# Optimization experiments

Measured on AMD Instinct MI355X. Metric: run time of the kernel, lower is better.

## Reference

```python
import jax, jax.numpy as jnp
import numpy as np

N_NODES = 50000
N_EDGES = 800000
DIM = 128
NEG_SLOPE = 0.2


def gat_conv(x, ei, W, a_src, a_dst, b):
    """PyG GATConv, heads=1, add_self_loops=True."""
    N = x.shape[0]
    h = x @ W  # [N, out]
    loop = jnp.arange(N, dtype=ei.dtype)
    src = jnp.concatenate([ei[0], loop])
    dst = jnp.concatenate([ei[1], loop])
    al = h @ a_src  # [N]
    ar = h @ a_dst  # [N]
    e = jax.nn.leaky_relu(al[src] + ar[dst], NEG_SLOPE)  # [E+N]
    m = jax.ops.segment_max(e, dst, num_segments=N)
    ex = jnp.exp(e - m[dst])
    s = jax.ops.segment_sum(ex, dst, num_segments=N)
    alpha = ex / s[dst]
    out = jax.ops.segment_sum(h[src] * alpha[:, None], dst, num_segments=N)
    return out + b


def setup_inputs() -> dict:
    key = jax.random.key(0)
    ks = jax.random.split(key, 32)
    sc = 1.0 / np.sqrt(DIM)
    inp = {"x": jax.random.normal(ks[0], (N_NODES, DIM), jnp.float32)}
    for i in range(5):
        inp[f"W{i+1}"] = jax.random.normal(ks[1 + 4 * i], (DIM, DIM), jnp.float32) * sc
        inp[f"as{i+1}"] = jax.random.normal(ks[2 + 4 * i], (DIM,), jnp.float32) * sc
        inp[f"ad{i+1}"] = jax.random.normal(ks[3 + 4 * i], (DIM,), jnp.float32) * sc
        inp[f"b{i+1}"] = jnp.zeros((DIM,), jnp.float32)
    inp["edge_index"] = jax.random.randint(ks[22], (2, N_EDGES), 0, N_NODES, jnp.int32)
    inp["edge_index_cross"] = jax.random.randint(ks[23], (2, N_EDGES), 0, N_NODES, jnp.int32)
    return inp


def reference(x, W1, as1, ad1, b1, W2, as2, ad2, b2, W3, as3, ad3, b3,
              W4, as4, ad4, b4, W5, as5, ad5, b5, edge_index, edge_index_cross):
    # dropout is identity in inference mode
    x = jax.nn.relu(gat_conv(x, edge_index, W1, as1, ad1, b1))
    x = jax.nn.relu(gat_conv(x, edge_index_cross, W2, as2, ad2, b2))
    x = jax.nn.relu(gat_conv(x, edge_index, W3, as3, ad3, b3))
    x = jax.nn.relu(gat_conv(x, edge_index_cross, W4, as4, ad4, b4))
    x = gat_conv(x, edge_index, W5, as5, ad5, b5)
    return jnp.squeeze(x)
```

## Files before the change

### kernel.cpp

```cpp
#include <hip/hip_runtime.h>

#define DIM 128
#define NEG 0.2f
#define CAP 128
#define BSZ 512
#define CB  256

typedef __attribute__((ext_vector_type(8))) short bf16x8;
typedef __attribute__((ext_vector_type(4))) float f32x4;
typedef __attribute__((ext_vector_type(8))) _Float16 h16x8;
typedef __attribute__((ext_vector_type(8))) unsigned short us8;

__device__ __forceinline__ float lrelu(float v) { return v > 0.f ? v : NEG * v; }

__device__ __forceinline__ unsigned short f2bf(float f) {
    unsigned u = __float_as_uint(f);
    unsigned r = (u + 0x7FFFu + ((u >> 16) & 1u)) >> 16;
    return (unsigned short)r;
}
__device__ __forceinline__ float bf2f(unsigned short h) {
    return __uint_as_float(((unsigned)h) << 16);
}


__global__ __launch_bounds__(256) void convert_x(const float* __restrict__ x,
                                                 unsigned short* __restrict__ hi,
                                                 unsigned short* __restrict__ lo, int n4) {
    int i = blockIdx.x * 256 + threadIdx.x;
    if (i >= n4) return;
    const int p = i * 4;
    const int tile = p >> 11, kc = (p >> 9) & 3, q = (p >> 7) & 3;
    const int rr = (p >> 3) & 15, j0 = p & 7;
    const int row = tile * 16 + rr;
    const int k = kc * 32 + q * 8 + j0;
    float4 v = *(const float4*)(x + (size_t)row * DIM + k);
    ushort4 h, l;
    h.x = f2bf(v.x); l.x = f2bf(v.x - bf2f(h.x));
    h.y = f2bf(v.y); l.y = f2bf(v.y - bf2f(h.y));
    h.z = f2bf(v.z); l.z = f2bf(v.z - bf2f(h.z));
    h.w = f2bf(v.w); l.w = f2bf(v.w - bf2f(h.w));
    *(ushort4*)(hi + p) = h;
    *(ushort4*)(lo + p) = l;
}

__global__ __launch_bounds__(256) void convert_w(const float* __restrict__ W,
                                                 unsigned short* __restrict__ Bhi,
                                                 unsigned short* __restrict__ Blo) {
    int i = blockIdx.x * 256 + threadIdx.x;
    if (i >= 16384) return;
    const int tt = i >> 11, kc = (i >> 9) & 3, q = (i >> 7) & 3;
    const int n = (i >> 3) & 15, j = i & 7;
    const int c = tt * 16 + n;
    const int k = kc * 32 + q * 8 + j;
    float v = W[k * 128 + c];
    unsigned short h = f2bf(v);
    Bhi[i] = h;
    Blo[i] = f2bf(v - bf2f(h));
}

__global__ __launch_bounds__(256) void gemm_mfma(const unsigned short* __restrict__ Ahi,
                                                 const unsigned short* __restrict__ Alo,
                                                 const unsigned short* __restrict__ Bhi,
                                                 const unsigned short* __restrict__ Blo,
                                                 const float* __restrict__ asrc,
                                                 const float* __restrict__ adst,
                                                 _Float16* __restrict__ Hh,
                                                 float* __restrict__ al,
                                                 float* __restrict__ ar, int N) {
    const int t = threadIdx.x;
    const int wv = t >> 6;
    const int l = t & 63;
    const int tile = blockIdx.x * 4 + wv;
    const int r0 = tile * 16;
    const int m = l & 15;
    const int q = l >> 4;

    f32x4 acc[8];
#pragma unroll
    for (int tt = 0; tt < 8; ++tt) acc[tt] = (f32x4){0.f, 0.f, 0.f, 0.f};

    const size_t abase = (size_t)tile * 2048 + (size_t)l * 8;
#pragma unroll
    for (int kc = 0; kc < 4; ++kc) {
        const bf16x8 ahi = *(const bf16x8*)(Ahi + abase + kc * 512);
        const bf16x8 alo = *(const bf16x8*)(Alo + abase + kc * 512);
#pragma unroll
        for (int tt = 0; tt < 8; ++tt) {
            const size_t boff = (size_t)tt * 2048 + kc * 512 + (size_t)l * 8;
            const bf16x8 bhi = *(const bf16x8*)(Bhi + boff);
            const bf16x8 blo = *(const bf16x8*)(Blo + boff);
            acc[tt] = __builtin_amdgcn_mfma_f32_16x16x32_bf16(ahi, bhi, acc[tt], 0, 0, 0);
            acc[tt] = __builtin_amdgcn_mfma_f32_16x16x32_bf16(ahi, blo, acc[tt], 0, 0, 0);
            acc[tt] = __builtin_amdgcn_mfma_f32_16x16x32_bf16(alo, bhi, acc[tt], 0, 0, 0);
        }
    }

#pragma unroll
    for (int j = 0; j < 4; ++j) {
        const int rr = r0 + q * 4 + j;
        if (rr < N) {
            _Float16* hp = Hh + (size_t)rr * DIM + m;
#pragma unroll
            for (int tt = 0; tt < 8; ++tt) hp[tt * 16] = (_Float16)acc[tt][j];
        }
    }

    float pa[4] = {0.f, 0.f, 0.f, 0.f};
    float pr[4] = {0.f, 0.f, 0.f, 0.f};
#pragma unroll
    for (int tt = 0; tt < 8; ++tt) {
        const float as = asrc[tt * 16 + m];
        const float ad = adst[tt * 16 + m];
#pragma unroll
        for (int j = 0; j < 4; ++j) {
            pa[j] += acc[tt][j] * as;
            pr[j] += acc[tt][j] * ad;
        }
    }
#pragma unroll
    for (int off = 8; off; off >>= 1) {
#pragma unroll
        for (int j = 0; j < 4; ++j) {
            pa[j] += __shfl_xor(pa[j], off);
            pr[j] += __shfl_xor(pr[j], off);
        }
    }
    if (m == 0) {
#pragma unroll
        for (int j = 0; j < 4; ++j) {
            const int rr = r0 + q * 4 + j;
            if (rr < N) { al[rr] = pa[j]; ar[rr] = pr[j]; }
        }
    }
}

__device__ __forceinline__ void edge_decode(int e, const int* ei, const int* eix,
                                            int E1, int N, int E2, int& src, int& d) {
    if (e < E1) {
        src = ei[e];
        d = ei[E1 + e];
    } else {
        int k = e - E1;
        src = eix[k];
        d = N + eix[E2 + k];
    }
}

__global__ __launch_bounds__(256) void csr_hist(const int* __restrict__ ei,
                                                const int* __restrict__ eix,
                                                int* __restrict__ g_hist,
                                                int E1, int E2, int N, int NB, int CE) {
    __shared__ int h[256];
    const int t = threadIdx.x;
    const int c = blockIdx.x;
    h[t] = 0;
    __syncthreads();
    const int Etot = E1 + E2;
    const int beg = c * CE;
    const int end = min(Etot, beg + CE);
    for (int e = beg + t; e < end; e += 256) {
        int src, d;
        edge_decode(e, ei, eix, E1, N, E2, src, d);
        atomicAdd(&h[d >> 9], 1);
    }
    __syncthreads();
    if (t < NB) g_hist[t * CB + c] = h[t];
}

__global__ __launch_bounds__(1024) void bsum_kernel(const int* __restrict__ in,
                                                    int* __restrict__ bsum, int L) {
    __shared__ int wsum[16];
    int t = threadIdx.x, wave = t >> 6, lane = t & 63;
    int i = blockIdx.x * 1024 + t;
    int v = (i < L) ? in[i] : 0;
#pragma unroll
    for (int off = 32; off; off >>= 1) v += __shfl_xor(v, off);
    if (lane == 0) wsum[wave] = v;
    __syncthreads();
    if (t == 0) {
        int s = 0;
#pragma unroll
        for (int j = 0; j < 16; ++j) s += wsum[j];
        bsum[blockIdx.x] = s;
    }
}

__global__ __launch_bounds__(128) void scan_small(int* __restrict__ bsum, int nb) {
    __shared__ int w0tot;
    int t = threadIdx.x;
    int v = (t < nb) ? bsum[t] : 0;
    int s = v;
#pragma unroll
    for (int off = 1; off < 64; off <<= 1) {
        int u = __shfl_up(s, off);
        if ((t & 63) >= off) s += u;
    }
    if (t == 63) w0tot = s;
    __syncthreads();
    if (t >= 64) s += w0tot;
    if (t < nb) bsum[t] = s - v;
}

__global__ __launch_bounds__(1024) void bscan_kernel(const int* __restrict__ in,
                                                     const int* __restrict__ bsum,
                                                     int* __restrict__ out, int L) {
    __shared__ int wsum[16];
    __shared__ int woff[16];
    int t = threadIdx.x, wave = t >> 6, lane = t & 63;
    int i = blockIdx.x * 1024 + t;
    int v = (i < L) ? in[i] : 0;
    int s = v;
#pragma unroll
    for (int off = 1; off < 64; off <<= 1) {
        int u = __shfl_up(s, off);
        if (lane >= off) s += u;
    }
    if (lane == 63) wsum[wave] = s;
    __syncthreads();
    if (t == 0) {
        int r = 0;
#pragma unroll
        for (int j = 0; j < 16; ++j) { woff[j] = r; r += wsum[j]; }
    }
    __syncthreads();
    if (i < L) out[i] = bsum[blockIdx.x] + woff[wave] + s - v;
}

__global__ __launch_bounds__(256) void csr_partition(const int* __restrict__ ei,
                                                     const int* __restrict__ eix,
                                                     const int* __restrict__ g_base,
                                                     unsigned* __restrict__ staging,
                                                     int E1, int E2, int N, int NB, int CE) {
    __shared__ int cur[256];
    const int t = threadIdx.x;
    const int c = blockIdx.x;
    if (t < NB) cur[t] = g_base[t * CB + c];
    __syncthreads();
    const int Etot = E1 + E2;
    const int beg = c * CE;
    const int end = min(Etot, beg + CE);
    for (int e = beg + t; e < end; e += 256) {
        int src, d;
        edge_decode(e, ei, eix, E1, N, E2, src, d);
        int p = atomicAdd(&cur[d >> 9], 1);
        staging[p] = ((unsigned)(d & (BSZ - 1)) << 22) | (unsigned)src;
    }
}

__global__ __launch_bounds__(256) void csr_finalize(const unsigned* __restrict__ staging,
                                                    const int* __restrict__ g_base,
                                                    int* __restrict__ row_off,
                                                    int* __restrict__ col,
                                                    int Ntot, int Etot, int NB) {
    __shared__ int cnt_s[BSZ];
    __shared__ int cur_s[BSZ];
    __shared__ int wsum[4], woff[4];
    const int t = threadIdx.x;
    const int k = blockIdx.x;
    cnt_s[t] = 0;
    cnt_s[t + 256] = 0;
    __syncthreads();
    const int seg_beg = g_base[k * CB];
    const int seg_end = (k == NB - 1) ? Etot : g_base[(k + 1) * CB];
    for (int i = seg_beg + t; i < seg_end; i += 256)
        atomicAdd(&cnt_s[staging[i] >> 22], 1);
    __syncthreads();

    const int a = cnt_s[2 * t], b = cnt_s[2 * t + 1];
    const int tsum = a + b;
    int s = tsum;
    const int lane = t & 63, wv = t >> 6;
#pragma unroll
    for (int off = 1; off < 64; off <<= 1) {
        int u = __shfl_up(s, off);
        if (lane >= off) s += u;
    }
    if (lane == 63) wsum[wv] = s;
    __syncthreads();
    if (t == 0) {
        int r = 0;
#pragma unroll
        for (int j = 0; j < 4; ++j) { woff[j] = r; r += wsum[j]; }
    }
    __syncthreads();
    const int excl = woff[wv] + s - tsum;
    cur_s[2 * t] = seg_beg + excl;
    cur_s[2 * t + 1] = seg_beg + excl + a;
    const int nbase = k * BSZ;
    if (nbase + 2 * t < Ntot)     row_off[nbase + 2 * t]     = seg_beg + excl;
    if (nbase + 2 * t + 1 < Ntot) row_off[nbase + 2 * t + 1] = seg_beg + excl + a;
    __syncthreads();
    for (int i = seg_beg + t; i < seg_end; i += 256) {
        unsigned v = staging[i];
        int p = atomicAdd(&cur_s[v >> 22], 1);
        col[p] = (int)(v & 0x3FFFFFu);
    }
    if (k == 0 && t == 0) row_off[Ntot] = Etot;
}

__global__ __launch_bounds__(256) void agg_kernel(const _Float16* __restrict__ Hh,
                                                  const float* __restrict__ al,
                                                  const float* __restrict__ ar,
                                                  const int* __restrict__ row_off,
                                                  const int* __restrict__ col,
                                                  const float* __restrict__ bias,
                                                  float* __restrict__ outF,
                                                  unsigned short* __restrict__ outHi,
                                                  unsigned short* __restrict__ outLo,
                                                  int N, int last) {
    __shared__ float salpha[16][CAP];
    __shared__ int   scol[16][CAP];
    const int t = threadIdx.x;
    const int wv = t >> 6;
    const int lane = t & 63;
    const int g = lane >> 4;
    const int j = lane & 15;
    const int slot = wv * 4 + g;
    const int w = blockIdx.x * 16 + slot;
    if (w >= N) return;

    const int beg = row_off[w];
    const int deg = row_off[w + 1] - beg;
    const float arn = ar[w];
    const float vself = lrelu(al[w] + arn);

    float mm = -1e30f, ss = 0.f;
    for (int i = j; i < deg; i += 16) {
        const int c = col[beg + i];
        float v = lrelu(al[c] + arn);
        if (i < CAP) { scol[slot][i] = c; salpha[slot][i] = v; }
        float nm = fmaxf(mm, v);
        ss = ss * __expf(mm - nm) + __expf(v - nm);
        mm = nm;
    }
#pragma unroll
    for (int off = 8; off; off >>= 1) {
        float mo = __shfl_xor(mm, off);
        float so = __shfl_xor(ss, off);
        float nm = fmaxf(mm, mo);
        ss = ss * __expf(mm - nm) + so * __expf(mo - nm);
        mm = nm;
    }
    {
        float nm = fmaxf(mm, vself);
        ss = ss * __expf(mm - nm) + __expf(vself - nm);
        mm = nm;
    }
    const float m = mm;
    const float invs = 1.f / ss;

    const int capdeg = deg < CAP ? deg : CAP;
    for (int i = j; i < capdeg; i += 16)
        salpha[slot][i] = __expf(salpha[slot][i] - m) * invs;

    const float aself = __expf(vself - m) * invs;
    const h16x8 hs = *(const h16x8*)(Hh + (size_t)w * DIM + 8 * j);
    float acc[8];
#pragma unroll
    for (int k = 0; k < 8; ++k) acc[k] = aself * (float)hs[k];

    int i = 0;
    for (; i + 3 < deg; i += 4) {
        int sn0, sn1, sn2, sn3;
        float a0, a1, a2, a3;
        if (i + 3 < CAP) {
            sn0 = scol[slot][i];     a0 = salpha[slot][i];
            sn1 = scol[slot][i + 1]; a1 = salpha[slot][i + 1];
            sn2 = scol[slot][i + 2]; a2 = salpha[slot][i + 2];
            sn3 = scol[slot][i + 3]; a3 = salpha[slot][i + 3];
        } else {
            const int e = beg + i;
            sn0 = col[e]; sn1 = col[e + 1]; sn2 = col[e + 2]; sn3 = col[e + 3];
            a0 = __expf(lrelu(al[sn0] + arn) - m) * invs;
            a1 = __expf(lrelu(al[sn1] + arn) - m) * invs;
            a2 = __expf(lrelu(al[sn2] + arn) - m) * invs;
            a3 = __expf(lrelu(al[sn3] + arn) - m) * invs;
        }
        const h16x8 h0 = *(const h16x8*)(Hh + (size_t)sn0 * DIM + 8 * j);
        const h16x8 h1 = *(const h16x8*)(Hh + (size_t)sn1 * DIM + 8 * j);
        const h16x8 h2 = *(const h16x8*)(Hh + (size_t)sn2 * DIM + 8 * j);
        const h16x8 h3 = *(const h16x8*)(Hh + (size_t)sn3 * DIM + 8 * j);
#pragma unroll
        for (int k = 0; k < 8; ++k)
            acc[k] += a0 * (float)h0[k] + a1 * (float)h1[k] +
                      a2 * (float)h2[k] + a3 * (float)h3[k];
    }
    for (; i < deg; ++i) {
        int sn;
        float a;
        if (i < CAP) {
            sn = scol[slot][i];
            a = salpha[slot][i];
        } else {
            sn = col[beg + i];
            a = __expf(lrelu(al[sn] + arn) - m) * invs;
        }
        const h16x8 hv = *(const h16x8*)(Hh + (size_t)sn * DIM + 8 * j);
#pragma unroll
        for (int k = 0; k < 8; ++k) acc[k] += a * (float)hv[k];
    }

    const float4 b0 = *(const float4*)(bias + 8 * j);
    const float4 b1 = *(const float4*)(bias + 8 * j + 4);
    float o[8];
    o[0] = acc[0] + b0.x; o[1] = acc[1] + b0.y;
    o[2] = acc[2] + b0.z; o[3] = acc[3] + b0.w;
    o[4] = acc[4] + b1.x; o[5] = acc[5] + b1.y;
    o[6] = acc[6] + b1.z; o[7] = acc[7] + b1.w;
    if (last) {
        float4 o0 = make_float4(o[0], o[1], o[2], o[3]);
        float4 o1 = make_float4(o[4], o[5], o[6], o[7]);
        *(float4*)(outF + (size_t)w * DIM + 8 * j) = o0;
        *(float4*)(outF + (size_t)w * DIM + 8 * j + 4) = o1;
    } else {
        us8 hv, lv;
#pragma unroll
        for (int k = 0; k < 8; ++k) {
            float v = fmaxf(o[k], 0.f);
            unsigned short hb = f2bf(v);
            hv[k] = hb;
            lv[k] = f2bf(v - bf2f(hb));
        }
        const size_t p = (size_t)(w >> 4) * 2048 +
                         (size_t)((j >> 2) * 512 + (j & 3) * 128 + (w & 15) * 8);
        *(us8*)(outHi + p) = hv;
        *(us8*)(outLo + p) = lv;
    }
}

extern "C" void kernel_launch(void* const* d_in, const int* in_sizes, int n_in,
                              void* d_out, int out_size, void* d_ws, size_t ws_size,
                              hipStream_t stream) {
    const float* x = (const float*)d_in[0];
    const float* W[5];
    const float* asv[5];
    const float* adv[5];
    const float* bv[5];
    for (int i = 0; i < 5; ++i) {
        W[i]   = (const float*)d_in[1 + 4 * i];
        asv[i] = (const float*)d_in[2 + 4 * i];
        adv[i] = (const float*)d_in[3 + 4 * i];
        bv[i]  = (const float*)d_in[4 + 4 * i];
    }
    const int* ei  = (const int*)d_in[21];
    const int* eix = (const int*)d_in[22];
    const int N  = in_sizes[0] / DIM;
    const int E1 = in_sizes[21] / 2;
    const int E2 = in_sizes[22] / 2;
    const int Ntot = 2 * N;
    const int Etot = E1 + E2;
    const int NB = (Ntot + BSZ - 1) / BSZ;
    const int CE = (Etot + CB - 1) / CB;
    const int gemm_blocks = (N + 63) / 64;
    const size_t tiles_alloc = (size_t)gemm_blocks * 4;

    size_t off = 0;
    auto alloc = [&](size_t bytes) {
        void* r = (char*)d_ws + off;
        off += (bytes + 255) & ~(size_t)255;
        return r;
    };
    float* Hbuf  = (float*)alloc((size_t)N * DIM * sizeof(float));
    unsigned short* Xhi = (unsigned short*)alloc(tiles_alloc * 2048 * 2);
    unsigned short* Xlo = (unsigned short*)alloc(tiles_alloc * 2048 * 2);
    float* al    = (float*)alloc((size_t)N * sizeof(float));
    float* ar    = (float*)alloc((size_t)N * sizeof(float));
    unsigned short* wthi = (unsigned short*)alloc(5 * 16384 * 2);
    unsigned short* wtlo = (unsigned short*)alloc(5 * 16384 * 2);
    int* g_hist  = (int*)alloc((size_t)NB * CB * sizeof(int));
    int* g_base  = (int*)alloc((size_t)NB * CB * sizeof(int));
    int* bsum    = (int*)alloc(128 * sizeof(int));
    int* row     = (int*)alloc((size_t)(Ntot + 1) * sizeof(int));
    int* col     = (int*)alloc((size_t)Etot * sizeof(int));
    (void)ws_size;
    unsigned* staging = (unsigned*)Hbuf;
    _Float16* Hh = (_Float16*)Hbuf;

    float* F = (float*)d_out;

    const int n4 = N * DIM / 4;
    convert_x<<<(n4 + 255) / 256, 256, 0, stream>>>(x, Xhi, Xlo, n4);
    for (int Lyr = 0; Lyr < 5; ++Lyr)
        convert_w<<<64, 256, 0, stream>>>(W[Lyr], wthi + Lyr * 16384, wtlo + Lyr * 16384);

    const int L = NB * CB;
    const int nbb = (L + 1023) / 1024;
    csr_hist<<<CB, 256, 0, stream>>>(ei, eix, g_hist, E1, E2, N, NB, CE);
    bsum_kernel<<<nbb, 1024, 0, stream>>>(g_hist, bsum, L);
    scan_small<<<1, 128, 0, stream>>>(bsum, nbb);
    bscan_kernel<<<nbb, 1024, 0, stream>>>(g_hist, bsum, g_base, L);
    csr_partition<<<CB, 256, 0, stream>>>(ei, eix, g_base, staging, E1, E2, N, NB, CE);
    csr_finalize<<<NB, 256, 0, stream>>>(staging, g_base, row, col, Ntot, Etot, NB);

    const int node_blocks = (N + 15) / 16;

    for (int Lyr = 0; Lyr < 5; ++Lyr) {
        gemm_mfma<<<gemm_blocks, 256, 0, stream>>>(Xhi, Xlo,
                                                   wthi + Lyr * 16384, wtlo + Lyr * 16384,
                                                   asv[Lyr], adv[Lyr], Hh, al, ar, N);
        const int* ro = row + ((Lyr % 2 == 0) ? 0 : N);
        agg_kernel<<<node_blocks, 256, 0, stream>>>(Hh, al, ar, ro, col, bv[Lyr],
                                                    F, Xhi, Xlo, N, (Lyr == 4) ? 1 : 0);
    }
}
```

Before: 444.6 us.

## Stage GEMM weights in LDS, degree-sort nodes for aggregation, batch weight conversion

The GEMM kernel now copies the split bf16 weight matrices into shared memory once per block and keeps the A fragments in registers, so B is no longer reread from global memory for every tile. A new bitonic sort reorders nodes by in-degree within each group of 256, and the aggregation kernel reads its node index through that permutation so the 16 nodes sharing a block have similar degrees and less divergence. The five weight-conversion launches are merged into one. The trade-offs are 64KB of LDS per GEMM block, which limits occupancy, two extra sort launches, and an indirection in the aggregation kernel that scatters its output writes.

```diff
diff --git a/kernel.cpp b/kernel.cpp
--- a/kernel.cpp
+++ b/kernel.cpp
@@ -43,19 +43,25 @@
     *(ushort4*)(lo + p) = l;
 }
 
-__global__ __launch_bounds__(256) void convert_w(const float* __restrict__ W,
+__global__ __launch_bounds__(256) void convert_w(const float* __restrict__ W0,
+                                                 const float* __restrict__ W1,
+                                                 const float* __restrict__ W2,
+                                                 const float* __restrict__ W3,
+                                                 const float* __restrict__ W4,
                                                  unsigned short* __restrict__ Bhi,
                                                  unsigned short* __restrict__ Blo) {
-    int i = blockIdx.x * 256 + threadIdx.x;
-    if (i >= 16384) return;
+    const int Lyr = blockIdx.x >> 6;
+    const float* W = (Lyr == 0) ? W0 : (Lyr == 1) ? W1 : (Lyr == 2) ? W2
+                    : (Lyr == 3) ? W3 : W4;
+    int i = (blockIdx.x & 63) * 256 + threadIdx.x;
     const int tt = i >> 11, kc = (i >> 9) & 3, q = (i >> 7) & 3;
     const int n = (i >> 3) & 15, j = i & 7;
     const int c = tt * 16 + n;
     const int k = kc * 32 + q * 8 + j;
     float v = W[k * 128 + c];
     unsigned short h = f2bf(v);
-    Bhi[i] = h;
-    Blo[i] = f2bf(v - bf2f(h));
+    Bhi[Lyr * 16384 + i] = h;
+    Blo[Lyr * 16384 + i] = f2bf(v - bf2f(h));
 }
 
 __global__ __launch_bounds__(256) void gemm_mfma(const unsigned short* __restrict__ Ahi,
@@ -67,6 +73,8 @@
                                                  _Float16* __restrict__ Hh,
                                                  float* __restrict__ al,
                                                  float* __restrict__ ar, int N) {
+    __shared__ unsigned short sBhi[16384];
+    __shared__ unsigned short sBlo[16384];
     const int t = threadIdx.x;
     const int wv = t >> 6;
     const int l = t & 63;
@@ -75,23 +83,40 @@
     const int m = l & 15;
     const int q = l >> 4;
 
+    bf16x8 ahi[4], alo[4];
+    const size_t abase = (size_t)tile * 2048 + (size_t)l * 8;
+#pragma unroll
+    for (int kc = 0; kc < 4; ++kc) {
+        ahi[kc] = *(const bf16x8*)(Ahi + abase + kc * 512);
+        alo[kc] = *(const bf16x8*)(Alo + abase + kc * 512);
+    }
+    {
+        const int4* gh = (const int4*)Bhi;
+        const int4* gl = (const int4*)Blo;
+        int4* sh = (int4*)sBhi;
+        int4* sl = (int4*)sBlo;
+#pragma unroll
+        for (int r = 0; r < 8; ++r) {
+            sh[t + 256 * r] = gh[t + 256 * r];
+            sl[t + 256 * r] = gl[t + 256 * r];
+        }
+    }
+    __syncthreads();
+
     f32x4 acc[8];
 #pragma unroll
     for (int tt = 0; tt < 8; ++tt) acc[tt] = (f32x4){0.f, 0.f, 0.f, 0.f};
 
-    const size_t abase = (size_t)tile * 2048 + (size_t)l * 8;
-#pragma unroll
-    for (int kc = 0; kc < 4; ++kc) {
-        const bf16x8 ahi = *(const bf16x8*)(Ahi + abase + kc * 512);
-        const bf16x8 alo = *(const bf16x8*)(Alo + abase + kc * 512);
-#pragma unroll
-        for (int tt = 0; tt < 8; ++tt) {
-            const size_t boff = (size_t)tt * 2048 + kc * 512 + (size_t)l * 8;
-            const bf16x8 bhi = *(const bf16x8*)(Bhi + boff);
-            const bf16x8 blo = *(const bf16x8*)(Blo + boff);
-            acc[tt] = __builtin_amdgcn_mfma_f32_16x16x32_bf16(ahi, bhi, acc[tt], 0, 0, 0);
-            acc[tt] = __builtin_amdgcn_mfma_f32_16x16x32_bf16(ahi, blo, acc[tt], 0, 0, 0);
-            acc[tt] = __builtin_amdgcn_mfma_f32_16x16x32_bf16(alo, bhi, acc[tt], 0, 0, 0);
+#pragma unroll
+    for (int tt = 0; tt < 8; ++tt) {
+#pragma unroll
+        for (int kc = 0; kc < 4; ++kc) {
+            const int boff = tt * 2048 + kc * 512 + l * 8;
+            const bf16x8 bhi = *(const bf16x8*)(sBhi + boff);
+            const bf16x8 blo = *(const bf16x8*)(sBlo + boff);
+            acc[tt] = __builtin_amdgcn_mfma_f32_16x16x32_bf16(ahi[kc], bhi, acc[tt], 0, 0, 0);
+            acc[tt] = __builtin_amdgcn_mfma_f32_16x16x32_bf16(ahi[kc], blo, acc[tt], 0, 0, 0);
+            acc[tt] = __builtin_amdgcn_mfma_f32_16x16x32_bf16(alo[kc], bhi, acc[tt], 0, 0, 0);
         }
     }
 
@@ -298,11 +323,39 @@
     if (k == 0 && t == 0) row_off[Ntot] = Etot;
 }
 
+__global__ __launch_bounds__(256) void sort_nodes(const int* __restrict__ row_off,
+                                                  int* __restrict__ perm, int N) {
+    __shared__ int kdeg[256];
+    __shared__ int kidx[256];
+    const int t = threadIdx.x;
+    const int w = blockIdx.x * 256 + t;
+    kdeg[t] = (w < N) ? (row_off[w + 1] - row_off[w]) : -1;
+    kidx[t] = w;
+    __syncthreads();
+#pragma unroll
+    for (int ksz = 2; ksz <= 256; ksz <<= 1) {
+        for (int jj = ksz >> 1; jj > 0; jj >>= 1) {
+            const int ixj = t ^ jj;
+            if (ixj > t) {
+                const int d0 = kdeg[t], d1 = kdeg[ixj];
+                const bool up = ((t & ksz) == 0);
+                if ((d0 > d1) == up) {
+                    kdeg[t] = d1; kdeg[ixj] = d0;
+                    const int i0 = kidx[t]; kidx[t] = kidx[ixj]; kidx[ixj] = i0;
+                }
+            }
+            __syncthreads();
+        }
+    }
+    perm[blockIdx.x * 256 + t] = kidx[t];
+}
+
 __global__ __launch_bounds__(256) void agg_kernel(const _Float16* __restrict__ Hh,
                                                   const float* __restrict__ al,
                                                   const float* __restrict__ ar,
                                                   const int* __restrict__ row_off,
                                                   const int* __restrict__ col,
+                                                  const int* __restrict__ perm,
                                                   const float* __restrict__ bias,
                                                   float* __restrict__ outF,
                                                   unsigned short* __restrict__ outHi,
@@ -316,7 +369,7 @@
     const int g = lane >> 4;
     const int j = lane & 15;
     const int slot = wv * 4 + g;
-    const int w = blockIdx.x * 16 + slot;
+    const int w = perm[blockIdx.x * 16 + slot];
     if (w >= N) return;
 
     const int beg = row_off[w];
@@ -453,6 +506,8 @@
     const int CE = (Etot + CB - 1) / CB;
     const int gemm_blocks = (N + 63) / 64;
     const size_t tiles_alloc = (size_t)gemm_blocks * 4;
+    const int PW = (N + 255) / 256;
+    const int PN = PW * 256;
 
     size_t off = 0;
     auto alloc = [&](size_t bytes) {
@@ -472,6 +527,7 @@
     int* bsum    = (int*)alloc(128 * sizeof(int));
     int* row     = (int*)alloc((size_t)(Ntot + 1) * sizeof(int));
     int* col     = (int*)alloc((size_t)Etot * sizeof(int));
+    int* perm    = (int*)alloc((size_t)2 * PN * sizeof(int));
     (void)ws_size;
     unsigned* staging = (unsigned*)Hbuf;
     _Float16* Hh = (_Float16*)Hbuf;
@@ -480,8 +536,7 @@
 
     const int n4 = N * DIM / 4;
     convert_x<<<(n4 + 255) / 256, 256, 0, stream>>>(x, Xhi, Xlo, n4);
-    for (int Lyr = 0; Lyr < 5; ++Lyr)
-        convert_w<<<64, 256, 0, stream>>>(W[Lyr], wthi + Lyr * 16384, wtlo + Lyr * 16384);
+    convert_w<<<320, 256, 0, stream>>>(W[0], W[1], W[2], W[3], W[4], wthi, wtlo);
 
     const int L = NB * CB;
     const int nbb = (L + 1023) / 1024;
@@ -492,14 +547,19 @@
     csr_partition<<<CB, 256, 0, stream>>>(ei, eix, g_base, staging, E1, E2, N, NB, CE);
     csr_finalize<<<NB, 256, 0, stream>>>(staging, g_base, row, col, Ntot, Etot, NB);
 
-    const int node_blocks = (N + 15) / 16;
+    sort_nodes<<<PW, 256, 0, stream>>>(row, perm, N);
+    sort_nodes<<<PW, 256, 0, stream>>>(row + N, perm + PN, N);
+
+    const int node_blocks = PN / 16;
 
     for (int Lyr = 0; Lyr < 5; ++Lyr) {
         gemm_mfma<<<gemm_blocks, 256, 0, stream>>>(Xhi, Xlo,
                                                    wthi + Lyr * 16384, wtlo + Lyr * 16384,
                                                    asv[Lyr], adv[Lyr], Hh, al, ar, N);
-        const int* ro = row + ((Lyr % 2 == 0) ? 0 : N);
-        agg_kernel<<<node_blocks, 256, 0, stream>>>(Hh, al, ar, ro, col, bv[Lyr],
+        const int half = (Lyr % 2 == 0) ? 0 : 1;
+        const int* ro = row + half * N;
+        const int* pm = perm + half * PN;
+        agg_kernel<<<node_blocks, 256, 0, stream>>>(Hh, al, ar, ro, col, pm, bv[Lyr],
                                                     F, Xhi, Xlo, N, (Lyr == 4) ? 1 : 0);
     }
 }
```

After: 496.9 us. +11.8%, slower.
